# Kernel optimization log

Measured on AMD Instinct MI355X. Metric: run time of the kernel, lower is better.

Reference implementation:

```python
import jax, jax.numpy as jnp
import numpy as np

H = 8          # n_heads
D_MODEL = 512
D_HEAD = 64    # d_keys = d_values = d_model // n_heads


def _fft_feats(x):
    # x: (B, L, C) real -> (B, C, L_fft, 3) stacking [real, imag, rfftfreq]
    n = x.shape[1]
    xf = jnp.fft.rfft(jnp.swapaxes(x, 1, 2), axis=-1)  # (B, C, L_fft) complex
    freqs = jnp.fft.rfftfreq(n).astype(x.dtype)        # (L_fft,)
    f = jnp.broadcast_to(freqs, xf.shape)
    return jnp.stack([xf.real.astype(x.dtype), xf.imag.astype(x.dtype), f], axis=-1)


def _proj_heads(feats, W, b):
    # Conv1d(kernel=3, stride=3) over the flattened (L_fft*3) axis is exactly a
    # per-frequency contraction over the 3 stacked features.
    # feats: (B, C, F, 3), W: (O, C, 3), b: (O,) -> (B, F, H, O//H)
    y = jnp.einsum('bcfk,ock->bfo', feats, W) + b
    B, F, O = y.shape
    return y.reshape(B, F, H, O // H)


def setup_inputs() -> dict:
    key = jax.random.key(0)
    ks = jax.random.split(key, 8)
    B, L, S = 16, 2048, 2048
    q = jax.random.normal(ks[0], (B, L, D_MODEL), jnp.float32)
    k = jax.random.normal(ks[1], (B, S, D_MODEL), jnp.float32)
    v = jax.random.normal(ks[2], (B, S, D_MODEL), jnp.float32)
    O = H * D_HEAD
    s = 1.0 / np.sqrt(3.0 * D_MODEL)
    Wq = jax.random.normal(ks[3], (O, D_MODEL, 3), jnp.float32) * s
    Wk = jax.random.normal(ks[4], (O, D_MODEL, 3), jnp.float32) * s
    Wv = jax.random.normal(ks[5], (O, D_MODEL, 3), jnp.float32) * s
    bq = jnp.zeros((O,), jnp.float32)
    bk = jnp.zeros((O,), jnp.float32)
    bv = jnp.zeros((O,), jnp.float32)
    Wo = jax.random.normal(ks[6], (2 * D_MODEL, O), jnp.float32) * (1.0 / np.sqrt(O))
    bo = jnp.zeros((2 * D_MODEL,), jnp.float32)
    return {"queries": q, "keys": k, "values": v,
            "Wq": Wq, "bq": bq, "Wk": Wk, "bk": bk, "Wv": Wv, "bv": bv,
            "Wo": Wo, "bo": bo}


def reference(queries, keys, values, Wq, bq, Wk, bk, Wv, bv, Wo, bo):
    B, L, _ = queries.shape
    qh = _proj_heads(_fft_feats(queries), Wq, bq)  # (B, Lf, H, E)
    kh = _proj_heads(_fft_feats(keys), Wk, bk)     # (B, Sf, H, E)
    vh = _proj_heads(_fft_feats(values), Wv, bv)   # (B, Sf, H, D)
    scale = 1.0 / jnp.sqrt(jnp.asarray(qh.shape[-1], qh.dtype))
    scores = jnp.einsum('blhe,bshe->bhls', qh, kh)
    attn = jax.nn.softmax(scale * scores, axis=-1)  # (B, H, Lf, Sf)
    ctx = jnp.einsum('bhls,bshd->blhd', attn, vh)   # (B, Lf, H, D)
    Lf = ctx.shape[1]
    ctx = ctx.reshape(B, Lf, H * D_HEAD)
    y = ctx @ Wo.T + bo                              # (B, Lf, 2*d_model)
    y = y.reshape(B, Lf, D_MODEL, 2)
    yc = jax.lax.complex(y[..., 0], y[..., 1])       # (B, Lf, d_model)
    out = jnp.fft.irfft(jnp.swapaxes(yc, 1, 2), n=L, axis=-1)  # (B, d_model, L)
    return jnp.swapaxes(out, 1, 2), attn
```

## Files before the change

### kernel.cpp

```cpp
#include <hip/hip_runtime.h>
#include <math.h>

#define FL 1025

typedef __bf16 bf16x8 __attribute__((ext_vector_type(8)));
typedef float  f32x4  __attribute__((ext_vector_type(4)));

static __device__ __forceinline__ bf16x8 ldfrag(const __bf16* p) {
  union { uint4 q; bf16x8 v; } u;
  u.q = *(const uint4*)p;
  return u.v;
}
static __device__ __forceinline__ float fexp(float x) { return __expf(x); }

static __device__ __forceinline__ unsigned pack_hl(float v) {
  __bf16 h = (__bf16)v;
  float hf = (float)h;
  __bf16 l = (__bf16)(v - hf);
  unsigned short uh, ul;
  __builtin_memcpy(&uh, &h, 2);
  __builtin_memcpy(&ul, &l, 2);
  return (unsigned)uh | ((unsigned)ul << 16);
}

static __device__ __forceinline__ void fft2048_stages(float* re, float* im, int tid, int dir) {
  for (int len = 2; len <= 2048; len <<= 1) {
    int half = len >> 1;
    __syncthreads();
    for (int t = tid; t < 1024; t += 256) {
      int j  = t & (half - 1);
      int i0 = ((t & ~(half - 1)) << 1) | j;
      int i1 = i0 + half;
      float ang = (2.0f * (float)j) / (float)len;
      float wr = cospif(ang);
      float s  = sinpif(ang);
      float wi = (dir > 0) ? s : -s;
      float vr = re[i1], vi = im[i1];
      float tr = vr * wr - vi * wi;
      float ti = vr * wi + vi * wr;
      float ur = re[i0], ui = im[i0];
      re[i0] = ur + tr; im[i0] = ui + ti;
      re[i1] = ur - tr; im[i1] = ui - ti;
    }
  }
  __syncthreads();
}

__global__ __launch_bounds__(256) void rfft3_kernel(const float* __restrict__ xT,
                                                    unsigned* __restrict__ QF3) {
  __shared__ float re[2048];
  __shared__ float im[2048];
  int c2 = blockIdx.x, b = blockIdx.y, t = blockIdx.z, tid = threadIdx.x;
  const float* pa = xT + (((long long)t * 16 + b) * 512 + 2 * c2) * 2048;
  const float* pb = pa + 2048;
  float4 a0 = *(const float4*)(pa + tid * 8);
  float4 a1 = *(const float4*)(pa + tid * 8 + 4);
  float4 b0 = *(const float4*)(pb + tid * 8);
  float4 b1 = *(const float4*)(pb + tid * 8 + 4);
  float va[8] = {a0.x, a0.y, a0.z, a0.w, a1.x, a1.y, a1.z, a1.w};
  float vb[8] = {b0.x, b0.y, b0.z, b0.w, b1.x, b1.y, b1.z, b1.w};
#pragma unroll
  for (int j = 0; j < 8; j++) {
    int l = tid * 8 + j;
    int r = __brev((unsigned)l) >> 21;
    re[r] = va[j];
    im[r] = vb[j];
  }
  fft2048_stages(re, im, tid, -1);
  unsigned* base = QF3 + ((long long)t * 16 + b) * 1052672;
  for (int f = tid; f <= 1024; f += 256) {
    int g = (2048 - f) & 2047;
    float fr = re[f], fi = im[f], gr = re[g], gi = im[g];
    float Xar = 0.5f * (fr + gr), Xai = 0.5f * (fi - gi);
    float Xbr = 0.5f * (fi + gi), Xbi = 0.5f * (gr - fr);
    base[(long long)(2 * c2) * 1028 + f]       = pack_hl(Xar);
    base[(long long)(512 + 2 * c2) * 1028 + f] = pack_hl(Xai);
    base[(long long)(2 * c2 + 1) * 1028 + f]   = pack_hl(Xbr);
    base[(long long)(513 + 2 * c2) * 1028 + f] = pack_hl(Xbi);
  }
}

__global__ __launch_bounds__(256) void irfft3_kernel(const float* __restrict__ ybT,
                                                     float* __restrict__ out) {
  __shared__ float Yar[FL], Yai[FL], Ybr[FL], Ybi[FL];
  __shared__ float re[2048];
  __shared__ float im[2048];
  int lin = blockIdx.y * 256 + blockIdx.x;
  int w = (lin & 7) * 512 + (lin >> 3);
  int d2 = w & 255;
  int b = w >> 8;
  int tid = threadIdx.x;
  const float* yp = ybT + ((long long)b * 1024 + 4 * d2) * 1025;
  for (int f = tid; f <= 1024; f += 256) {
    Yar[f] = yp[f];
    Yai[f] = yp[1025 + f];
    Ybr[f] = yp[2050 + f];
    Ybi[f] = yp[3075 + f];
  }
  __syncthreads();
  if (tid == 0) { Yai[0] = 0.f; Yai[1024] = 0.f; Ybi[0] = 0.f; Ybi[1024] = 0.f; }
  __syncthreads();
  for (int i = tid; i < 2048; i += 256) {
    int j = __brev((unsigned)i) >> 21;
    float rr, ii;
    if (j <= 1024) { rr = Yar[j] - Ybi[j]; ii = Yai[j] + Ybr[j]; }
    else { int f = 2048 - j; rr = Yar[f] + Ybi[f]; ii = Ybr[f] - Yai[f]; }
    re[i] = rr; im[i] = ii;
  }
  fft2048_stages(re, im, tid, +1);
  float* op = out + (long long)b * 2048 * 512 + 2 * d2;
  const float sc = 1.0f / 2048.0f;
  for (int l = tid; l < 2048; l += 256) {
    float2 v = {re[l] * sc, im[l] * sc};
    *(float2*)(op + (long long)l * 512) = v;
  }
}

__global__ __launch_bounds__(256) void transpose_x(const float* __restrict__ q,
                                                   const float* __restrict__ k,
                                                   const float* __restrict__ v,
                                                   float* __restrict__ xT) {
  __shared__ float t[32][33];
  int z = blockIdx.z;
  int ti = z >> 4, b = z & 15;
  const float* x = (ti == 0) ? q : (ti == 1) ? k : v;
  int l0 = blockIdx.x * 32, c0 = blockIdx.y * 32;
  int tx = threadIdx.x & 31, ty = threadIdx.x >> 5;
  for (int i = ty; i < 32; i += 8)
    t[i][tx] = x[((long long)b * 2048 + l0 + i) * 512 + c0 + tx];
  __syncthreads();
  float* dst = xT + ((long long)ti * 16 + b) * 512 * 2048;
  for (int i = ty; i < 32; i += 8)
    dst[((long long)(c0 + i)) * 2048 + l0 + tx] = t[tx][i];
}

__global__ __launch_bounds__(256) void setup_pack(
    const float* __restrict__ Wq, const float* __restrict__ Wk,
    const float* __restrict__ Wv, const float* __restrict__ Wo,
    const float* __restrict__ bq, const float* __restrict__ bk,
    const float* __restrict__ bv,
    __bf16* __restrict__ Wth, __bf16* __restrict__ Wtl,
    __bf16* __restrict__ Woh, float* __restrict__ wf3, float* __restrict__ bias3) {
  int bx = blockIdx.x, tid = threadIdx.x;
  if (bx < 6144) {
    int e = bx * 256 + tid;
    int t = e >> 19, local = e & 524287;
    const float* W = (t == 0) ? Wq : (t == 1) ? Wk : Wv;
    int o = local >> 10, kk = local & 1023;
    int c = kk & 511, j = kk >> 9;
    float v = W[(long long)o * 1536 + c * 3 + j];
    __bf16 h = (__bf16)v;
    Wth[e] = h;
    Wtl[e] = (__bf16)(v - (float)h);
  } else if (bx < 8192) {
    int e = (bx - 6144) * 256 + tid;
    Woh[e] = (__bf16)Wo[e];
  } else if (bx < 8198) {
    int idx = (bx - 8192) * 256 + tid;
    int t = idx / 512, o = idx & 511;
    const float* W = (t == 0) ? Wq : (t == 1) ? Wk : Wv;
    float s = 0.f;
    for (int c = 0; c < 512; c++) s += W[(long long)o * 1536 + c * 3 + 2];
    wf3[idx] = s;
  } else {
    int idx = (bx - 8198) * 256 + tid;
    int t = idx / 512, o = idx & 511;
    bias3[idx] = (t == 0) ? bq[o] : (t == 1) ? bk[o] : bv[o];
  }
}

__global__ __launch_bounds__(256) void proj_gemm(
    const unsigned* __restrict__ QF3,
    const __bf16* __restrict__ Wth, const __bf16* __restrict__ Wtl,
    const float* __restrict__ wf3, const float* __restrict__ bias3,
    __bf16* __restrict__ qhh, __bf16* __restrict__ qhl,
    __bf16* __restrict__ khh, __bf16* __restrict__ khl,
    __bf16* __restrict__ vhT, float uscale) {
  __shared__ __bf16 As[2][128][40];
  __shared__ __bf16 Bs[2][128][40];
  int tid = threadIdx.x;
  int wid = tid >> 6, lane = tid & 63;
  int lrow = lane & 15, quad = lane >> 4;
  int lin = (blockIdx.z * 4 + blockIdx.y) * 9 + blockIdx.x;
  int w = (lin & 7) * 216 + (lin >> 3);
  int m0 = (w % 9) * 128;
  int rem = w / 9;
  int n0 = (rem & 3) * 128;
  int z = rem >> 2;
  int t = z >> 4, b = z & 15;
  const unsigned* Ab = QF3 + (long long)z * 1052672;
  const __bf16* Bbh = Wth + (long long)t * 524288;
  const __bf16* Bbl = Wtl + (long long)t * 524288;

  int wm0 = (wid & 1) * 64, wn0 = (wid >> 1) * 64;
  int floc = tid & 127;
  int kg = (tid >> 7) * 4;
  const unsigned* Acol = Ab + min(m0 + floc, 1024);
  int srow = tid >> 1, shalf = tid & 1;

  f32x4 acc[4][4];
#pragma unroll
  for (int i = 0; i < 4; i++)
#pragma unroll
    for (int j = 0; j < 4; j++) acc[i][j] = (f32x4){0.f, 0.f, 0.f, 0.f};

  for (int k0 = 0; k0 < 1024; k0 += 32) {
#pragma unroll
    for (int it = 0; it < 4; it++) {
      int kko = kg + it * 8;
      unsigned u0 = Acol[(long long)(k0 + kko + 0) * 1028];
      unsigned u1 = Acol[(long long)(k0 + kko + 1) * 1028];
      unsigned u2 = Acol[(long long)(k0 + kko + 2) * 1028];
      unsigned u3 = Acol[(long long)(k0 + kko + 3) * 1028];
      uint2 hu = make_uint2((u0 & 0xffffu) | (u1 << 16),
                            (u2 & 0xffffu) | (u3 << 16));
      uint2 lu = make_uint2((u0 >> 16) | (u1 & 0xffff0000u),
                            (u2 >> 16) | (u3 & 0xffff0000u));
      *(uint2*)&As[0][floc][kko] = hu;
      *(uint2*)&As[1][floc][kko] = lu;
    }
    {
      const __bf16* s = Bbh + (long long)(n0 + srow) * 1024 + k0 + shalf * 16;
      uint4* d = (uint4*)&Bs[0][srow][shalf * 16];
      d[0] = ((const uint4*)s)[0]; d[1] = ((const uint4*)s)[1];
      s = Bbl + (long long)(n0 + srow) * 1024 + k0 + shalf * 16;
      d = (uint4*)&Bs[1][srow][shalf * 16];
      d[0] = ((const uint4*)s)[0]; d[1] = ((const uint4*)s)[1];
    }
    __syncthreads();

    bf16x8 bh[4], bl[4];
#pragma unroll
    for (int nt = 0; nt < 4; nt++) {
      int r = wn0 + nt * 16 + lrow;
      bh[nt] = ldfrag(&Bs[0][r][quad * 8]);
      bl[nt] = ldfrag(&Bs[1][r][quad * 8]);
    }
#pragma unroll
    for (int mt = 0; mt < 4; mt++) {
      int r = wm0 + mt * 16 + lrow;
      bf16x8 ah = ldfrag(&As[0][r][quad * 8]);
      bf16x8 al = ldfrag(&As[1][r][quad * 8]);
#pragma unroll
      for (int nt = 0; nt < 4; nt++) {
        acc[mt][nt] = __builtin_amdgcn_mfma_f32_16x16x32_bf16(ah, bh[nt], acc[mt][nt], 0, 0, 0);
        acc[mt][nt] = __builtin_amdgcn_mfma_f32_16x16x32_bf16(ah, bl[nt], acc[mt][nt], 0, 0, 0);
        acc[mt][nt] = __builtin_amdgcn_mfma_f32_16x16x32_bf16(al, bh[nt], acc[mt][nt], 0, 0, 0);
      }
    }
    __syncthreads();
  }

  __bf16* Ch = (t == 0) ? qhh : khh;
  __bf16* Cl = (t == 0) ? qhl : khl;
#pragma unroll
  for (int mt = 0; mt < 4; mt++) {
#pragma unroll
    for (int nt = 0; nt < 4; nt++) {
      int gn = n0 + wn0 + nt * 16 + lrow;
      float bn = bias3[t * 512 + gn];
      float vn = wf3[t * 512 + gn];
      int gmb = m0 + wm0 + mt * 16 + quad * 4;
      if (t < 2) {
#pragma unroll
        for (int r = 0; r < 4; r++) {
          int gm = gmb + r;
          if (gm < FL) {
            float val = acc[mt][nt][r] + bn + uscale * (float)gm * vn;
            long long o = ((long long)b * FL + gm) * 512 + gn;
            __bf16 h = (__bf16)val;
            Ch[o] = h;
            Cl[o] = (__bf16)(val - (float)h);
          }
        }
      } else {
        int hh = gn >> 6, dd = gn & 63;
        long long ob = ((long long)(b * 8 + hh) * 64 + dd) * 1152;
#pragma unroll
        for (int r = 0; r < 4; r++) {
          int gm = gmb + r;
          if (gm < FL) {
            float val = acc[mt][nt][r] + bn + uscale * (float)gm * vn;
            vhT[ob + gm] = (__bf16)val;
          }
        }
      }
    }
  }
}

__global__ __launch_bounds__(256) void oproj_gemm(
    const __bf16* __restrict__ ctx, const __bf16* __restrict__ Woh,
    const float* __restrict__ bo, float* __restrict__ ybT) {
  __shared__ __bf16 As[128][40];
  __shared__ __bf16 Bs[128][40];
  int tid = threadIdx.x;
  int wid = tid >> 6, lane = tid & 63;
  int lrow = lane & 15, quad = lane >> 4;
  int lin = (blockIdx.z * 8 + blockIdx.y) * 9 + blockIdx.x;
  int w = (lin & 7) * 144 + (lin >> 3);
  int m0 = (w % 9) * 128;
  int rem = w / 9;
  int n0 = (rem & 7) * 128;
  int z = rem >> 3;
  const __bf16* Ab = ctx + (long long)z * 524800;
  int wm0 = (wid & 1) * 64, wn0 = (wid >> 1) * 64;
  int srow = tid >> 1, shalf = tid & 1;
  int arow = min(m0 + srow, FL - 1);

  f32x4 acc[4][4];
#pragma unroll
  for (int i = 0; i < 4; i++)
#pragma unroll
    for (int j = 0; j < 4; j++) acc[i][j] = (f32x4){0.f, 0.f, 0.f, 0.f};

  for (int k0 = 0; k0 < 512; k0 += 32) {
    {
      const __bf16* s = Ab + (long long)arow * 512 + k0 + shalf * 16;
      uint4* d = (uint4*)&As[srow][shalf * 16];
      d[0] = ((const uint4*)s)[0]; d[1] = ((const uint4*)s)[1];
      s = Woh + (long long)(n0 + srow) * 512 + k0 + shalf * 16;
      d = (uint4*)&Bs[srow][shalf * 16];
      d[0] = ((const uint4*)s)[0]; d[1] = ((const uint4*)s)[1];
    }
    __syncthreads();
    bf16x8 bh[4];
#pragma unroll
    for (int nt = 0; nt < 4; nt++) bh[nt] = ldfrag(&Bs[wn0 + nt * 16 + lrow][quad * 8]);
#pragma unroll
    for (int mt = 0; mt < 4; mt++) {
      bf16x8 ah = ldfrag(&As[wm0 + mt * 16 + lrow][quad * 8]);
#pragma unroll
      for (int nt = 0; nt < 4; nt++)
        acc[mt][nt] = __builtin_amdgcn_mfma_f32_16x16x32_bf16(ah, bh[nt], acc[mt][nt], 0, 0, 0);
    }
    __syncthreads();
  }

#pragma unroll
  for (int mt = 0; mt < 4; mt++) {
#pragma unroll
    for (int nt = 0; nt < 4; nt++) {
      int gn = n0 + wn0 + nt * 16 + lrow;
      float bn = bo[gn];
      int gmb = m0 + wm0 + mt * 16 + quad * 4;
      long long ob = (long long)z * 1049600 + (long long)gn * 1025;
#pragma unroll
      for (int r = 0; r < 4; r++) {
        int gm = gmb + r;
        if (gm < FL) ybT[ob + gm] = acc[mt][nt][r] + bn;
      }
    }
  }
}

static __device__ __forceinline__ void compute_S_tile(
    const __bf16 (*Kh)[72], const __bf16 (*Kl)[72],
    const bf16x8 (&qf)[2][2], int lrow, int quad, int n0, f32x4* sa) {
#pragma unroll
  for (int nt = 0; nt < 8; nt++) sa[nt] = (f32x4){0.f, 0.f, 0.f, 0.f};
#pragma unroll
  for (int kit = 0; kit < 2; kit++) {
#pragma unroll
    for (int nt = 0; nt < 8; nt++) {
      bf16x8 kh = ldfrag(&Kh[nt * 16 + lrow][kit * 32 + quad * 8]);
      bf16x8 kl = ldfrag(&Kl[nt * 16 + lrow][kit * 32 + quad * 8]);
      sa[nt] = __builtin_amdgcn_mfma_f32_16x16x32_bf16(qf[0][kit], kh, sa[nt], 0, 0, 0);
      sa[nt] = __builtin_amdgcn_mfma_f32_16x16x32_bf16(qf[0][kit], kl, sa[nt], 0, 0, 0);
      sa[nt] = __builtin_amdgcn_mfma_f32_16x16x32_bf16(qf[1][kit], kh, sa[nt], 0, 0, 0);
    }
  }
#pragma unroll
  for (int nt = 0; nt < 8; nt++) {
    int gn = n0 + nt * 16 + lrow;
    bool ok = gn < FL;
#pragma unroll
    for (int r = 0; r < 4; r++) sa[nt][r] = ok ? sa[nt][r] * 0.125f : -INFINITY;
  }
}

__global__ __launch_bounds__(512) void flash_kernel(
    const __bf16* __restrict__ qh_h, const __bf16* __restrict__ qh_l,
    const __bf16* __restrict__ kh_h, const __bf16* __restrict__ kh_l,
    const __bf16* __restrict__ vhT,
    float* __restrict__ attn, __bf16* __restrict__ ctxb) {
  __shared__ __align__(16) char smem[54272];
  __bf16 (*Kh)[72]  = (__bf16 (*)[72])smem;
  __bf16 (*Kl)[72]  = (__bf16 (*)[72])(smem + 18432);
  __bf16 (*P)[136]  = (__bf16 (*)[136])smem;
  __bf16 (*Bv)[136] = (__bf16 (*)[136])(smem + 36864);

  int tid = threadIdx.x;
  int wid = tid >> 6, lane = tid & 63;
  int lrow = lane & 15, quad = lane >> 4;
  int lin = blockIdx.z * 9 + blockIdx.x;
  int w = (lin & 7) * 144 + (lin >> 3);
  int f0 = (w % 9) * 128;
  int z = w / 9;
  int b = z >> 3, h = z & 7;

  bf16x8 qf[2][2];
  {
    int rowq = min(f0 + wid * 16 + lrow, FL - 1);
    long long base = ((long long)b * FL + rowq) * 512 + h * 64 + quad * 8;
#pragma unroll
    for (int kit = 0; kit < 2; kit++) {
      qf[0][kit] = ldfrag(qh_h + base + kit * 32);
      qf[1][kit] = ldfrag(qh_l + base + kit * 32);
    }
  }

  int sp = tid >> 8, srw = (tid >> 1) & 127, shalf = tid & 1;
  const __bf16* ksrc0 = (sp ? kh_l : kh_h) + (long long)b * FL * 512 + h * 64 + shalf * 32;
  __bf16* kdst = (sp ? Kl[srw] : Kh[srw]) + shalf * 32;

  float m_i[4], l_i[4];
#pragma unroll
  for (int r = 0; r < 4; r++) { m_i[r] = -INFINITY; l_i[r] = 0.f; }

  f32x4 sa[8];

  for (int nt0 = 0; nt0 < 9; nt0++) {
    __syncthreads();
    {
      int srowg = min(nt0 * 128 + srw, FL - 1);
      const __bf16* s = ksrc0 + (long long)srowg * 512;
#pragma unroll
      for (int u = 0; u < 4; u++) ((uint4*)kdst)[u] = ((const uint4*)s)[u];
    }
    __syncthreads();
    compute_S_tile(Kh, Kl, qf, lrow, quad, nt0 * 128, sa);
#pragma unroll
    for (int r = 0; r < 4; r++) {
      float mx = -INFINITY;
#pragma unroll
      for (int nt = 0; nt < 8; nt++) mx = fmaxf(mx, sa[nt][r]);
      for (int o = 1; o < 16; o <<= 1) mx = fmaxf(mx, __shfl_xor(mx, o, 64));
      float mn = fmaxf(m_i[r], mx);
      float al = fexp(m_i[r] - mn);
      float ps = 0.f;
#pragma unroll
      for (int nt = 0; nt < 8; nt++) ps += fexp(sa[nt][r] - mn);
      for (int o = 1; o < 16; o <<= 1) ps += __shfl_xor(ps, o, 64);
      l_i[r] = l_i[r] * al + ps;
      m_i[r] = mn;
    }
  }

  float rl[4];
#pragma unroll
  for (int r = 0; r < 4; r++) rl[r] = 1.0f / l_i[r];

  f32x4 oa[4];
#pragma unroll
  for (int j = 0; j < 4; j++) oa[j] = (f32x4){0.f, 0.f, 0.f, 0.f};

  int vrow = tid >> 3, voff = (tid & 7) * 16;
  const __bf16* vsrc0 = vhT + ((long long)z * 64 + vrow) * 1152 + voff;
  __bf16* vdst = &Bv[vrow][voff];

  float* attnz = attn + (long long)z * 1050625;
  for (int nt0 = 0; nt0 < 9; nt0++) {
    __syncthreads();
    {
      int srowg = min(nt0 * 128 + srw, FL - 1);
      const __bf16* s = ksrc0 + (long long)srowg * 512;
#pragma unroll
      for (int u = 0; u < 4; u++) ((uint4*)kdst)[u] = ((const uint4*)s)[u];
      const __bf16* vs = vsrc0 + nt0 * 128;
      ((uint4*)vdst)[0] = ((const uint4*)vs)[0];
      ((uint4*)vdst)[1] = ((const uint4*)vs)[1];
    }
    __syncthreads();
    compute_S_tile(Kh, Kl, qf, lrow, quad, nt0 * 128, sa);
    __syncthreads();
#pragma unroll
    for (int nt = 0; nt < 8; nt++) {
      int gn = nt0 * 128 + nt * 16 + lrow;
#pragma unroll
      for (int r = 0; r < 4; r++) {
        float p = fexp(sa[nt][r] - m_i[r]) * rl[r];
        int lm = wid * 16 + quad * 4 + r;
        int gm = f0 + lm;
        if (gm < FL && gn < FL) attnz[(long long)gm * FL + gn] = p;
        P[lm][nt * 16 + lrow] = (__bf16)p;
      }
    }
#pragma unroll
    for (int kk = 0; kk < 4; kk++) {
      bf16x8 pf = ldfrag(&P[wid * 16 + lrow][kk * 32 + quad * 8]);
#pragma unroll
      for (int nto = 0; nto < 4; nto++) {
        bf16x8 vf = ldfrag(&Bv[nto * 16 + lrow][kk * 32 + quad * 8]);
        oa[nto] = __builtin_amdgcn_mfma_f32_16x16x32_bf16(pf, vf, oa[nto], 0, 0, 0);
      }
    }
  }

#pragma unroll
  for (int nto = 0; nto < 4; nto++) {
#pragma unroll
    for (int r = 0; r < 4; r++) {
      int gm = f0 + wid * 16 + quad * 4 + r;
      if (gm < FL)
        ctxb[((long long)b * FL + gm) * 512 + h * 64 + nto * 16 + lrow] = (__bf16)oa[nto][r];
    }
  }
}

extern "C" void kernel_launch(void* const* d_in, const int* in_sizes, int n_in,
                              void* d_out, int out_size, void* d_ws, size_t ws_size,
                              hipStream_t stream) {
  (void)in_sizes; (void)n_in; (void)out_size; (void)ws_size;
  const float* q  = (const float*)d_in[0];
  const float* k  = (const float*)d_in[1];
  const float* v  = (const float*)d_in[2];
  const float* Wq = (const float*)d_in[3];
  const float* bq = (const float*)d_in[4];
  const float* Wk = (const float*)d_in[5];
  const float* bk = (const float*)d_in[6];
  const float* Wv = (const float*)d_in[7];
  const float* bv = (const float*)d_in[8];
  const float* Wo = (const float*)d_in[9];
  const float* bo = (const float*)d_in[10];

  float* outp = (float*)d_out;
  float* attn = outp + (long long)16 * 2048 * 512;

  float* ws = (float*)d_ws;
  float*  xT   = ws;
  float*  QF3  = xT + 50331648;
  float*  wf3  = QF3 + 50528256;
  float*  bias3= wf3 + 1536;
  __bf16* Wth  = (__bf16*)(bias3 + 1536);
  __bf16* Wtl  = Wth + 1572864;
  __bf16* Woh  = Wtl + 1572864;
  __bf16* qhh  = Woh + 524288;
  __bf16* qhl  = qhh + 8396800;
  __bf16* khh  = qhl + 8396800;
  __bf16* khl  = khh + 8396800;
  __bf16* vhT  = khl + 8396800;
  __bf16* ctx  = (__bf16*)QF3;
  float*  ybT  = xT;

  transpose_x<<<dim3(64, 16, 48), 256, 0, stream>>>(q, k, v, xT);
  setup_pack<<<dim3(8204, 1, 1), 256, 0, stream>>>(Wq, Wk, Wv, Wo, bq, bk, bv,
                                                   Wth, Wtl, Woh, wf3, bias3);
  rfft3_kernel<<<dim3(256, 16, 3), 256, 0, stream>>>(xT, (unsigned*)QF3);

  proj_gemm<<<dim3(9, 4, 48), 256, 0, stream>>>(
      (const unsigned*)QF3, Wth, Wtl, wf3, bias3, qhh, qhl, khh, khl, vhT,
      1.0f / 2048.0f);

  flash_kernel<<<dim3(9, 1, 128), 512, 0, stream>>>(
      qhh, qhl, khh, khl, vhT, attn, ctx);

  oproj_gemm<<<dim3(9, 8, 16), 256, 0, stream>>>(ctx, Woh, bo, ybT);

  irfft3_kernel<<<dim3(256, 16), 256, 0, stream>>>(ybT, outp);
}
```

Measured before the change: 1.680 ms.

## Pre-transpose FFT features into split bf16 row-major layout for projection GEMM

Adds a transpose kernel that turns the packed hi/lo FFT feature matrix into two separate row-major bf16 arrays, plus a side buffer for the Nyquist row. The projection GEMM can then load its A tiles with contiguous vector loads instead of strided scalar loads and bit unpacking. The attn and irfft output stores also become nontemporal. The cost is an extra kernel launch and an extra round trip of the feature matrix through global memory, and it reuses the xT workspace.

```diff
diff --git a/kernel.cpp b/kernel.cpp
--- a/kernel.cpp
+++ b/kernel.cpp
@@ -5,6 +5,7 @@
 
 typedef __bf16 bf16x8 __attribute__((ext_vector_type(8)));
 typedef float  f32x4  __attribute__((ext_vector_type(4)));
+typedef float  f32x2  __attribute__((ext_vector_type(2)));
 
 static __device__ __forceinline__ bf16x8 ldfrag(const __bf16* p) {
   union { uint4 q; bf16x8 v; } u;
@@ -21,6 +22,9 @@
   __builtin_memcpy(&uh, &h, 2);
   __builtin_memcpy(&ul, &l, 2);
   return (unsigned)uh | ((unsigned)ul << 16);
+}
+static __device__ __forceinline__ __bf16 bits_bf16(unsigned short u) {
+  __bf16 h; __builtin_memcpy(&h, &u, 2); return h;
 }
 
 static __device__ __forceinline__ void fft2048_stages(float* re, float* im, int tid, int dir) {
@@ -77,6 +81,35 @@
     base[(long long)(512 + 2 * c2) * 1028 + f] = pack_hl(Xai);
     base[(long long)(2 * c2 + 1) * 1028 + f]   = pack_hl(Xbr);
     base[(long long)(513 + 2 * c2) * 1028 + f] = pack_hl(Xbi);
+  }
+}
+
+__global__ __launch_bounds__(256) void transpose_qf(const unsigned* __restrict__ QF3,
+                                                    __bf16* __restrict__ Ath,
+                                                    __bf16* __restrict__ Atl,
+                                                    __bf16* __restrict__ AtN) {
+  __shared__ unsigned t[64][65];
+  int z = blockIdx.z;
+  int f0 = blockIdx.x * 64, k0 = blockIdx.y * 64;
+  const unsigned* src = QF3 + (long long)z * 1052672;
+  if (f0 < 1024) {
+    int tx = threadIdx.x & 63, ty = threadIdx.x >> 6;
+    for (int i = ty; i < 64; i += 4)
+      t[i][tx] = src[(long long)(k0 + i) * 1028 + f0 + tx];
+    __syncthreads();
+    for (int j = ty; j < 64; j += 4) {
+      unsigned v = t[tx][j];
+      long long o = ((long long)z * 1024 + f0 + j) * 1024 + k0 + tx;
+      Ath[o] = bits_bf16((unsigned short)(v & 0xffffu));
+      Atl[o] = bits_bf16((unsigned short)(v >> 16));
+    }
+  } else {
+    if (threadIdx.x < 64) {
+      int i = threadIdx.x;
+      unsigned v = src[(long long)(k0 + i) * 1028 + 1024];
+      AtN[((long long)z * 2 + 0) * 1024 + k0 + i] = bits_bf16((unsigned short)(v & 0xffffu));
+      AtN[((long long)z * 2 + 1) * 1024 + k0 + i] = bits_bf16((unsigned short)(v >> 16));
+    }
   }
 }
 
@@ -111,8 +144,8 @@
   float* op = out + (long long)b * 2048 * 512 + 2 * d2;
   const float sc = 1.0f / 2048.0f;
   for (int l = tid; l < 2048; l += 256) {
-    float2 v = {re[l] * sc, im[l] * sc};
-    *(float2*)(op + (long long)l * 512) = v;
+    f32x2 v = {re[l] * sc, im[l] * sc};
+    __builtin_nontemporal_store(v, (f32x2*)(op + (long long)l * 512));
   }
 }
 
@@ -170,7 +203,8 @@
 }
 
 __global__ __launch_bounds__(256) void proj_gemm(
-    const unsigned* __restrict__ QF3,
+    const __bf16* __restrict__ Ath, const __bf16* __restrict__ Atl,
+    const __bf16* __restrict__ AtN,
     const __bf16* __restrict__ Wth, const __bf16* __restrict__ Wtl,
     const float* __restrict__ wf3, const float* __restrict__ bias3,
     __bf16* __restrict__ qhh, __bf16* __restrict__ qhl,
@@ -188,15 +222,22 @@
   int n0 = (rem & 3) * 128;
   int z = rem >> 2;
   int t = z >> 4, b = z & 15;
-  const unsigned* Ab = QF3 + (long long)z * 1052672;
   const __bf16* Bbh = Wth + (long long)t * 524288;
   const __bf16* Bbl = Wtl + (long long)t * 524288;
 
   int wm0 = (wid & 1) * 64, wn0 = (wid >> 1) * 64;
-  int floc = tid & 127;
-  int kg = (tid >> 7) * 4;
-  const unsigned* Acol = Ab + min(m0 + floc, 1024);
   int srow = tid >> 1, shalf = tid & 1;
+  const __bf16 *arh, *arl;
+  {
+    int fr = m0 + srow;
+    if (fr < 1024) {
+      arh = Ath + ((long long)z * 1024 + fr) * 1024;
+      arl = Atl + ((long long)z * 1024 + fr) * 1024;
+    } else {
+      arh = AtN + ((long long)z * 2 + 0) * 1024;
+      arl = AtN + ((long long)z * 2 + 1) * 1024;
+    }
+  }
 
   f32x4 acc[4][4];
 #pragma unroll
@@ -205,23 +246,15 @@
     for (int j = 0; j < 4; j++) acc[i][j] = (f32x4){0.f, 0.f, 0.f, 0.f};
 
   for (int k0 = 0; k0 < 1024; k0 += 32) {
-#pragma unroll
-    for (int it = 0; it < 4; it++) {
-      int kko = kg + it * 8;
-      unsigned u0 = Acol[(long long)(k0 + kko + 0) * 1028];
-      unsigned u1 = Acol[(long long)(k0 + kko + 1) * 1028];
-      unsigned u2 = Acol[(long long)(k0 + kko + 2) * 1028];
-      unsigned u3 = Acol[(long long)(k0 + kko + 3) * 1028];
-      uint2 hu = make_uint2((u0 & 0xffffu) | (u1 << 16),
-                            (u2 & 0xffffu) | (u3 << 16));
-      uint2 lu = make_uint2((u0 >> 16) | (u1 & 0xffff0000u),
-                            (u2 >> 16) | (u3 & 0xffff0000u));
-      *(uint2*)&As[0][floc][kko] = hu;
-      *(uint2*)&As[1][floc][kko] = lu;
-    }
     {
-      const __bf16* s = Bbh + (long long)(n0 + srow) * 1024 + k0 + shalf * 16;
-      uint4* d = (uint4*)&Bs[0][srow][shalf * 16];
+      const __bf16* s = arh + k0 + shalf * 16;
+      uint4* d = (uint4*)&As[0][srow][shalf * 16];
+      d[0] = ((const uint4*)s)[0]; d[1] = ((const uint4*)s)[1];
+      s = arl + k0 + shalf * 16;
+      d = (uint4*)&As[1][srow][shalf * 16];
+      d[0] = ((const uint4*)s)[0]; d[1] = ((const uint4*)s)[1];
+      s = Bbh + (long long)(n0 + srow) * 1024 + k0 + shalf * 16;
+      d = (uint4*)&Bs[0][srow][shalf * 16];
       d[0] = ((const uint4*)s)[0]; d[1] = ((const uint4*)s)[1];
       s = Bbl + (long long)(n0 + srow) * 1024 + k0 + shalf * 16;
       d = (uint4*)&Bs[1][srow][shalf * 16];
@@ -482,7 +515,8 @@
         float p = fexp(sa[nt][r] - m_i[r]) * rl[r];
         int lm = wid * 16 + quad * 4 + r;
         int gm = f0 + lm;
-        if (gm < FL && gn < FL) attnz[(long long)gm * FL + gn] = p;
+        if (gm < FL && gn < FL)
+          __builtin_nontemporal_store(p, &attnz[(long long)gm * FL + gn]);
         P[lm][nt * 16 + lrow] = (__bf16)p;
       }
     }
@@ -540,6 +574,9 @@
   __bf16* khh  = qhl + 8396800;
   __bf16* khl  = khh + 8396800;
   __bf16* vhT  = khl + 8396800;
+  __bf16* AtN  = vhT + 9437184;
+  __bf16* Ath  = (__bf16*)xT;
+  __bf16* Atl  = Ath + 50331648;
   __bf16* ctx  = (__bf16*)QF3;
   float*  ybT  = xT;
 
@@ -548,8 +585,10 @@
                                                    Wth, Wtl, Woh, wf3, bias3);
   rfft3_kernel<<<dim3(256, 16, 3), 256, 0, stream>>>(xT, (unsigned*)QF3);
 
+  transpose_qf<<<dim3(17, 16, 48), 256, 0, stream>>>((const unsigned*)QF3, Ath, Atl, AtN);
+
   proj_gemm<<<dim3(9, 4, 48), 256, 0, stream>>>(
-      (const unsigned*)QF3, Wth, Wtl, wf3, bias3, qhh, qhl, khh, khl, vhT,
+      Ath, Atl, AtN, Wth, Wtl, wf3, bias3, qhh, qhl, khh, khl, vhT,
       1.0f / 2048.0f);
 
   flash_kernel<<<dim3(9, 1, 128), 512, 0, stream>>>(
```

Measured after the change: 2.276 ms. +35.5%, slower.
